# Optimization experiments

Hardware: AMD Instinct MI355X
Metric: run time of the kernel (lower is better)

The kernel has to match this reference:

```python
import jax, jax.numpy as jnp
import numpy as np

NUM_PARTS = 16
NUM_K = 256          # num_k_per_part; table rows per part = NUM_K + 1
VAE_DIMS = 768
OUT_DIMS = 1024
B = 4096


def setup_inputs() -> dict:
    key = jax.random.key(0)
    k0, k1, k2, k3, k4 = jax.random.split(key, 5)
    hashes = jax.random.randint(k0, (B, NUM_PARTS), 0, NUM_K + 1)  # values 0..256
    # nn.init.normal_(embedding.weight, 0.0, 0.01)
    emb = jax.random.normal(k1, ((NUM_K + 1) * NUM_PARTS, VAE_DIMS), dtype=jnp.float32) * 0.01
    # projection: Linear(768 -> 1024), ReLU, Linear(1024 -> 1024)
    W1 = jax.random.normal(k2, (VAE_DIMS, OUT_DIMS), dtype=jnp.float32) * (1.0 / np.sqrt(VAE_DIMS))
    b1 = jnp.zeros((OUT_DIMS,), dtype=jnp.float32)
    W2 = jax.random.normal(k3, (OUT_DIMS, OUT_DIMS), dtype=jnp.float32) * (1.0 / np.sqrt(OUT_DIMS))
    b2 = jnp.zeros((OUT_DIMS,), dtype=jnp.float32)
    # pe = randn(num_parts, out_dims) * 1.0
    pe = jax.random.normal(k4, (NUM_PARTS, OUT_DIMS), dtype=jnp.float32)
    return {"hashes": hashes, "emb": emb, "W1": W1, "b1": b1, "W2": W2, "b2": b2, "pe": pe}


def reference(hashes, emb, W1, b1, W2, b2, pe):
    # forward(hashes, index=None, get_mu=False, input_is_mu=False)
    offset = jnp.arange(NUM_PARTS, dtype=hashes.dtype) * (NUM_K + 1)  # [P]
    idx = hashes + offset[None, :]                                    # [B, P]
    mu = emb[idx]                                                     # [B, P, VAE]
    h = jax.nn.relu(jnp.einsum('bpv,vh->bph', mu, W1) + b1)           # [B, P, OUT]
    projected = jnp.einsum('bph,ho->bpo', h, W2) + b2                 # [B, P, OUT]
    return projected + pe[None, :, :]                                 # pe broadcast over batch
```

## Files before the change

### kernel.cpp

```cpp
#include <hip/hip_runtime.h>
#include <stdint.h>

#define NPARTS 16
#define NK1    257
#define ROWS   4112
#define MPAD   4224
#define VAE    768
#define ODIM   1024
#define BROWS  65536

typedef __attribute__((ext_vector_type(4))) float f32x4;
typedef __attribute__((ext_vector_type(8))) short s16x8;

static __device__ __forceinline__ unsigned short f2bf(float f) {
  union { float f; unsigned u; } v; v.f = f;
  unsigned x = v.u;
  unsigned r = x + 0x7FFFu + ((x >> 16) & 1u);
  return (unsigned short)(r >> 16);
}

static __device__ __forceinline__ void gload_lds16(const void* g, void* l) {
  __builtin_amdgcn_global_load_lds(
      (const __attribute__((address_space(1))) unsigned int*)g,
      (__attribute__((address_space(3))) unsigned int*)l, 16, 0, 0);
}

#define EMB_BLOCKS 1024
__global__ __launch_bounds__(256) void prep_kernel(
    const float* __restrict__ emb, const float* __restrict__ W1,
    unsigned short* __restrict__ embB, unsigned short* __restrict__ w1t) {
  __shared__ unsigned short tile[32][33];
  const int tid = threadIdx.x;
  const int bid = blockIdx.x;
  if (bid < EMB_BLOCKS) {
    const int NQ = MPAD * VAE / 4;
    for (int g = bid * 256 + tid; g < NQ; g += EMB_BLOCKS * 256) {
      const int i4 = g * 4;
      ushort4 o;
      if (i4 < ROWS * VAE) {
        const float4 v = *(const float4*)(emb + i4);
        o.x = f2bf(v.x); o.y = f2bf(v.y); o.z = f2bf(v.z); o.w = f2bf(v.w);
      } else {
        o.x = 0; o.y = 0; o.z = 0; o.w = 0;
      }
      *(ushort4*)(embB + i4) = o;
    }
  } else {
    const int tb = bid - EMB_BLOCKS;
    const int nkt = VAE / 32;
    const int tk = (tb % nkt) * 32;
    const int tn = (tb / nkt) * 32;
    const int r  = tid >> 3;
    const int c4 = (tid & 7) * 4;
    const float4 v = *(const float4*)(W1 + (size_t)(tk + r) * ODIM + tn + c4);
    tile[r][c4 + 0] = f2bf(v.x);
    tile[r][c4 + 1] = f2bf(v.y);
    tile[r][c4 + 2] = f2bf(v.z);
    tile[r][c4 + 3] = f2bf(v.w);
    __syncthreads();
    ushort4 o;
    o.x = tile[c4 + 0][r];
    o.y = tile[c4 + 1][r];
    o.z = tile[c4 + 2][r];
    o.w = tile[c4 + 3][r];
    *(ushort4*)(w1t + (size_t)(tn + r) * VAE + tk + c4) = o;
  }
}

template <int K, int MODE, bool DO_W2T>
__global__ __launch_bounds__(256) void gemm_kernel(
    const unsigned short* __restrict__ A, const unsigned short* __restrict__ BT,
    const float* __restrict__ bias, const float* __restrict__ pe,
    unsigned short* __restrict__ outB, float* __restrict__ outF,
    const float* __restrict__ W2src, unsigned short* __restrict__ w2dst) {
  __shared__ __align__(16) unsigned short smem[2 * 12288];
  const int tid = threadIdx.x;

  if (DO_W2T && blockIdx.z == 1) {
    if (blockIdx.y >= 32) return;
    unsigned short (*tile)[132] = (unsigned short (*)[132])smem;
    const int tk = blockIdx.y * 32, tn = blockIdx.x * 128;
#pragma unroll
    for (int p = 0; p < 4; ++p) {
      const int row = (tid >> 5) + p * 8, c4 = (tid & 31) * 4;
      const float4 v = *(const float4*)(W2src + (size_t)(tk + row) * ODIM + tn + c4);
      tile[row][c4 + 0] = f2bf(v.x); tile[row][c4 + 1] = f2bf(v.y);
      tile[row][c4 + 2] = f2bf(v.z); tile[row][c4 + 3] = f2bf(v.w);
    }
    __syncthreads();
#pragma unroll
    for (int q = 0; q < 4; ++q) {
      const int n = (tid >> 3) + q * 32, k4 = (tid & 7) * 4;
      ushort4 o;
      o.x = tile[k4 + 0][n]; o.y = tile[k4 + 1][n];
      o.z = tile[k4 + 2][n]; o.w = tile[k4 + 3][n];
      *(ushort4*)(w2dst + (size_t)(tn + n) * ODIM + tk + k4) = o;
    }
    return;
  }

  const int lane = tid & 63;
  const int wave = tid >> 6;
  const int wc   = wave * 32;
  const int brow = blockIdx.y * 64;
  const int bcol = blockIdx.x * 128;
  const int la   = lane & 15;
  const int hi   = lane >> 4;

  f32x4 acc[4][2];
#pragma unroll
  for (int m = 0; m < 4; ++m)
#pragma unroll
    for (int n = 0; n < 2; ++n)
#pragma unroll
      for (int r = 0; r < 4; ++r) acc[m][n][r] = 0.f;

  const int srow = tid >> 3;
  const int skb  = (tid & 7) ^ (srow & 7);
  const unsigned short* gA = A + (size_t)(brow + srow) * K + skb * 8;
  const unsigned short* gB = BT + (size_t)(bcol + srow) * K + skb * 8;

#define STAGE(b, kt)                                              \
  {                                                               \
    unsigned short* la_ = smem + (b) * 12288 + tid * 8;           \
    unsigned short* lb_ = la_ + 4096;                             \
    gload_lds16(gA + (kt), la_);                                  \
    gload_lds16(gA + (kt) + 32 * K, la_ + 2048);                  \
    gload_lds16(gB + (kt), lb_);                                  \
    gload_lds16(gB + (kt) + 32 * K, lb_ + 2048);                  \
    gload_lds16(gB + (kt) + 64 * K, lb_ + 4096);                  \
    gload_lds16(gB + (kt) + 96 * K, lb_ + 6144);                  \
  }

  STAGE(0, 0);
  asm volatile("s_waitcnt vmcnt(0)" ::: "memory");
  __builtin_amdgcn_s_barrier();

  const int NT = K / 64;
  for (int t = 0; t < NT; ++t) {
    const int cur = t & 1;
    if (t + 1 < NT) STAGE(cur ^ 1, (t + 1) * 64);

    const unsigned short* As = smem + cur * 12288;
    const unsigned short* Bs = As + 4096;
    s16x8 af[4][2], bf[2][2];
#pragma unroll
    for (int m = 0; m < 4; ++m)
#pragma unroll
      for (int ks = 0; ks < 2; ++ks)
        af[m][ks] = *(const s16x8*)(As + (m * 16 + la) * 64 +
                                    (((ks * 4 + hi) ^ (la & 7)) * 8));
#pragma unroll
    for (int n = 0; n < 2; ++n)
#pragma unroll
      for (int ks = 0; ks < 2; ++ks)
        bf[n][ks] = *(const s16x8*)(Bs + (wc + n * 16 + la) * 64 +
                                    (((ks * 4 + hi) ^ (la & 7)) * 8));
#pragma unroll
    for (int m = 0; m < 4; ++m)
#pragma unroll
      for (int n = 0; n < 2; ++n)
#pragma unroll
        for (int ks = 0; ks < 2; ++ks)
          acc[m][n] = __builtin_amdgcn_mfma_f32_16x16x32_bf16(af[m][ks], bf[n][ks],
                                                              acc[m][n], 0, 0, 0);
    asm volatile("s_waitcnt vmcnt(0)" ::: "memory");
    __builtin_amdgcn_sched_barrier(0);
    __builtin_amdgcn_s_barrier();
  }
#undef STAGE

#pragma unroll
  for (int m = 0; m < 4; ++m) {
    const int row0 = brow + m * 16 + hi * 4;
#pragma unroll
    for (int n = 0; n < 2; ++n) {
      const int col = bcol + wc + n * 16 + la;
      const float bv = bias[col];
      if (MODE == 0) {
#pragma unroll
        for (int r = 0; r < 4; ++r) {
          float v = acc[m][n][r] + bv;
          v = v > 0.f ? v : 0.f;
          outB[(size_t)(row0 + r) * ODIM + col] = f2bf(v);
        }
      } else {
#pragma unroll
        for (int r = 0; r < 4; ++r) {
          const int row = row0 + r;
          int p = row / NK1;
          if (p > NPARTS - 1) p = NPARTS - 1;
          outF[(size_t)row * ODIM + col] = acc[m][n][r] + bv + pe[(size_t)p * ODIM + col];
        }
      }
    }
  }
}

__global__ __launch_bounds__(256) void gather_kernel(const int* __restrict__ hashes,
                                                     const float* __restrict__ T,
                                                     float* __restrict__ out) {
  const int wid  = (blockIdx.x * blockDim.x + threadIdx.x) >> 6;
  const int lane = threadIdx.x & 63;
  const int nw   = (gridDim.x * blockDim.x) >> 6;
  for (int row = wid; row < BROWS; row += nw) {
    const int h = __builtin_amdgcn_readfirstlane(hashes[row]);
    const int p = row & (NPARTS - 1);
    const f32x4* __restrict__ src = (const f32x4*)(T + (size_t)(h + p * NK1) * ODIM);
    f32x4* __restrict__ dst = (f32x4*)(out + (size_t)row * ODIM);
#pragma unroll
    for (int j = 0; j < 4; ++j) {
      f32x4 v = src[lane + j * 64];
      __builtin_nontemporal_store(v, dst + lane + j * 64);
    }
  }
}

extern "C" void kernel_launch(void* const* d_in, const int* in_sizes, int n_in,
                              void* d_out, int out_size, void* d_ws, size_t ws_size,
                              hipStream_t stream) {
  const int*   hashes = (const int*)d_in[0];
  const float* emb    = (const float*)d_in[1];
  const float* W1     = (const float*)d_in[2];
  const float* b1     = (const float*)d_in[3];
  const float* W2     = (const float*)d_in[4];
  const float* b2     = (const float*)d_in[5];
  const float* pe     = (const float*)d_in[6];
  float* out = (float*)d_out;

  char* ws = (char*)d_ws;
  unsigned short* embB = (unsigned short*)(ws);
  unsigned short* w1t  = (unsigned short*)(ws + 6488064);
  unsigned short* w2t  = (unsigned short*)(ws + 8060928);
  unsigned short* H    = (unsigned short*)(ws + 10158080);
  float*          T    = (float*)(ws + 18808832);

  prep_kernel<<<EMB_BLOCKS + 768, 256, 0, stream>>>(emb, W1, embB, w1t);

  gemm_kernel<VAE, 0, true><<<dim3(8, 66, 2), 256, 0, stream>>>(
      embB, w1t, b1, nullptr, H, nullptr, W2, w2t);

  gemm_kernel<ODIM, 2, false><<<dim3(8, 66, 1), 256, 0, stream>>>(
      H, w2t, b2, pe, nullptr, T, nullptr, nullptr);

  gather_kernel<<<1024, 256, 0, stream>>>(hashes, T, out);
}
```

Measured before the change: 94.00 us.

## Fuse table gather into second GEMM epilogue via per-part hash bucketing

Builds per-part histograms and a bucketed row list of batch rows for each table entry inside the prep kernel. The second GEMM stages its output tile in shared memory and scatters each table row directly to every output row that references it. This removes the intermediate fp32 table write and the separate gather kernel's reread of it. It adds atomics, prefix scans, a per-row binary search and scattered stores in the epilogue.

```diff
diff --git a/kernel.cpp b/kernel.cpp
--- a/kernel.cpp
+++ b/kernel.cpp
@@ -8,6 +8,7 @@
 #define VAE    768
 #define ODIM   1024
 #define BROWS  65536
+#define BPART  4096
 
 typedef __attribute__((ext_vector_type(4))) float f32x4;
 typedef __attribute__((ext_vector_type(8))) short s16x8;
@@ -26,10 +27,14 @@
 }
 
 #define EMB_BLOCKS 1024
+#define W1_BLOCKS  768
 __global__ __launch_bounds__(256) void prep_kernel(
     const float* __restrict__ emb, const float* __restrict__ W1,
-    unsigned short* __restrict__ embB, unsigned short* __restrict__ w1t) {
+    const int* __restrict__ hashes,
+    unsigned short* __restrict__ embB, unsigned short* __restrict__ w1t,
+    int* __restrict__ gcnt, int* __restrict__ gbase, int* __restrict__ rowlist) {
   __shared__ unsigned short tile[32][33];
+  __shared__ int hist[512];
   const int tid = threadIdx.x;
   const int bid = blockIdx.x;
   if (bid < EMB_BLOCKS) {
@@ -45,7 +50,7 @@
       }
       *(ushort4*)(embB + i4) = o;
     }
-  } else {
+  } else if (bid < EMB_BLOCKS + W1_BLOCKS) {
     const int tb = bid - EMB_BLOCKS;
     const int nkt = VAE / 32;
     const int tk = (tb % nkt) * 32;
@@ -64,6 +69,41 @@
     o.z = tile[c4 + 2][r];
     o.w = tile[c4 + 3][r];
     *(ushort4*)(w1t + (size_t)(tn + r) * VAE + tk + c4) = o;
+  } else {
+    const int p = bid - (EMB_BLOCKS + W1_BLOCKS);
+    hist[tid] = 0; hist[tid + 256] = 0;
+    __syncthreads();
+    int hv[16];
+#pragma unroll
+    for (int u = 0; u < 16; ++u) {
+      const int b = u * 256 + tid;
+      hv[u] = hashes[b * NPARTS + p];
+      atomicAdd(&hist[hv[u]], 1);
+    }
+    __syncthreads();
+    const int o0 = hist[tid], o1 = hist[tid + 256];
+    for (int off = 1; off < 512; off <<= 1) {
+      const int v0 = (tid >= off) ? hist[tid - off] : 0;
+      const int v1 = hist[tid + 256 - off];
+      __syncthreads();
+      hist[tid] += v0; hist[tid + 256] += v1;
+      __syncthreads();
+    }
+    const int b0 = hist[tid] - o0;
+    const int b1 = hist[tid + 256] - o1;
+    gcnt[p * NK1 + tid]  = o0;
+    gbase[p * NK1 + tid] = b0;
+    if (tid == 0) { gcnt[p * NK1 + 256] = o1; gbase[p * NK1 + 256] = b1; }
+    if (p == 0 && tid < MPAD - ROWS) { gcnt[ROWS + tid] = 0; gbase[ROWS + tid] = 0; }
+    __syncthreads();
+    hist[tid] = b0; hist[tid + 256] = b1;
+    __syncthreads();
+#pragma unroll
+    for (int u = 0; u < 16; ++u) {
+      const int b = u * 256 + tid;
+      const int pos = atomicAdd(&hist[hv[u]], 1);
+      rowlist[p * BPART + pos] = b * NPARTS + p;
+    }
   }
 }
 
@@ -72,28 +112,30 @@
     const unsigned short* __restrict__ A, const unsigned short* __restrict__ BT,
     const float* __restrict__ bias, const float* __restrict__ pe,
     unsigned short* __restrict__ outB, float* __restrict__ outF,
-    const float* __restrict__ W2src, unsigned short* __restrict__ w2dst) {
+    const float* __restrict__ W2src, unsigned short* __restrict__ w2dst,
+    const int* __restrict__ gcnt, const int* __restrict__ gbase,
+    const int* __restrict__ rowlist) {
   __shared__ __align__(16) unsigned short smem[2 * 12288];
   const int tid = threadIdx.x;
 
   if (DO_W2T && blockIdx.z == 1) {
     if (blockIdx.y >= 32) return;
-    unsigned short (*tile)[132] = (unsigned short (*)[132])smem;
+    unsigned short (*ttile)[132] = (unsigned short (*)[132])smem;
     const int tk = blockIdx.y * 32, tn = blockIdx.x * 128;
 #pragma unroll
-    for (int p = 0; p < 4; ++p) {
-      const int row = (tid >> 5) + p * 8, c4 = (tid & 31) * 4;
+    for (int q = 0; q < 4; ++q) {
+      const int row = (tid >> 5) + q * 8, c4 = (tid & 31) * 4;
       const float4 v = *(const float4*)(W2src + (size_t)(tk + row) * ODIM + tn + c4);
-      tile[row][c4 + 0] = f2bf(v.x); tile[row][c4 + 1] = f2bf(v.y);
-      tile[row][c4 + 2] = f2bf(v.z); tile[row][c4 + 3] = f2bf(v.w);
+      ttile[row][c4 + 0] = f2bf(v.x); ttile[row][c4 + 1] = f2bf(v.y);
+      ttile[row][c4 + 2] = f2bf(v.z); ttile[row][c4 + 3] = f2bf(v.w);
     }
     __syncthreads();
 #pragma unroll
     for (int q = 0; q < 4; ++q) {
       const int n = (tid >> 3) + q * 32, k4 = (tid & 7) * 4;
       ushort4 o;
-      o.x = tile[k4 + 0][n]; o.y = tile[k4 + 1][n];
-      o.z = tile[k4 + 2][n]; o.w = tile[k4 + 3][n];
+      o.x = ttile[k4 + 0][n]; o.y = ttile[k4 + 1][n];
+      o.z = ttile[k4 + 2][n]; o.w = ttile[k4 + 3][n];
       *(ushort4*)(w2dst + (size_t)(tn + n) * ODIM + tk + k4) = o;
     }
     return;
@@ -170,48 +212,70 @@
   }
 #undef STAGE
 
-#pragma unroll
-  for (int m = 0; m < 4; ++m) {
-    const int row0 = brow + m * 16 + hi * 4;
-#pragma unroll
-    for (int n = 0; n < 2; ++n) {
-      const int col = bcol + wc + n * 16 + la;
-      const float bv = bias[col];
-      if (MODE == 0) {
+  if constexpr (MODE == 0) {
+#pragma unroll
+    for (int m = 0; m < 4; ++m) {
+      const int row0 = brow + m * 16 + hi * 4;
+#pragma unroll
+      for (int n = 0; n < 2; ++n) {
+        const int col = bcol + wc + n * 16 + la;
+        const float bv = bias[col];
 #pragma unroll
         for (int r = 0; r < 4; ++r) {
           float v = acc[m][n][r] + bv;
           v = v > 0.f ? v : 0.f;
           outB[(size_t)(row0 + r) * ODIM + col] = f2bf(v);
         }
-      } else {
+      }
+    }
+  } else {
+    __shared__ int pref[65];
+    __shared__ int cbase[64];
+    float (*tile)[128] = (float (*)[128])smem;
+#pragma unroll
+    for (int m = 0; m < 4; ++m) {
+      const int trl = m * 16 + hi * 4;
+#pragma unroll
+      for (int n = 0; n < 2; ++n) {
+        const int lcol = wc + n * 16 + la;
+        const int gcol = bcol + lcol;
+        const float bv = bias[gcol];
 #pragma unroll
         for (int r = 0; r < 4; ++r) {
-          const int row = row0 + r;
-          int p = row / NK1;
-          if (p > NPARTS - 1) p = NPARTS - 1;
-          outF[(size_t)row * ODIM + col] = acc[m][n][r] + bv + pe[(size_t)p * ODIM + col];
+          const int trow = brow + trl + r;
+          int p = trow / NK1; if (p > NPARTS - 1) p = NPARTS - 1;
+          tile[trl + r][lcol] = acc[m][n][r] + bv + pe[(size_t)p * ODIM + gcol];
         }
       }
     }
-  }
-}
-
-__global__ __launch_bounds__(256) void gather_kernel(const int* __restrict__ hashes,
-                                                     const float* __restrict__ T,
-                                                     float* __restrict__ out) {
-  const int wid  = (blockIdx.x * blockDim.x + threadIdx.x) >> 6;
-  const int lane = threadIdx.x & 63;
-  const int nw   = (gridDim.x * blockDim.x) >> 6;
-  for (int row = wid; row < BROWS; row += nw) {
-    const int h = __builtin_amdgcn_readfirstlane(hashes[row]);
-    const int p = row & (NPARTS - 1);
-    const f32x4* __restrict__ src = (const f32x4*)(T + (size_t)(h + p * NK1) * ODIM);
-    f32x4* __restrict__ dst = (f32x4*)(out + (size_t)row * ODIM);
-#pragma unroll
-    for (int j = 0; j < 4; ++j) {
-      f32x4 v = src[lane + j * 64];
-      __builtin_nontemporal_store(v, dst + lane + j * 64);
+    if (wave == 0) {
+      const int trow = brow + lane;
+      const int c = gcnt[trow];
+      int s = c;
+#pragma unroll
+      for (int off = 1; off < 64; off <<= 1) {
+        const int v = __shfl_up(s, off);
+        if (lane >= off) s += v;
+      }
+      pref[lane + 1] = s;
+      if (lane == 0) pref[0] = 0;
+      int p = trow / NK1; if (p > NPARTS - 1) p = NPARTS - 1;
+      cbase[lane] = p * BPART + gbase[trow];
+    }
+    __syncthreads();
+    const int Nit = pref[64];
+    const int hw  = wave * 2 + (lane >> 5);
+    const int l32 = lane & 31;
+    for (int iq = hw; iq < Nit; iq += 8) {
+      int lo = 0, hh = 64;
+      while (hh - lo > 1) {
+        const int mid = (lo + hh) >> 1;
+        if (pref[mid] <= iq) lo = mid; else hh = mid;
+      }
+      const int t = lo;
+      const int orow = rowlist[cbase[t] + (iq - pref[t])];
+      const f32x4 v = *(const f32x4*)&tile[t][l32 * 4];
+      __builtin_nontemporal_store(v, (f32x4*)(outF + (size_t)orow * ODIM + bcol + l32 * 4));
     }
   }
 }
@@ -233,15 +297,16 @@
   unsigned short* w1t  = (unsigned short*)(ws + 6488064);
   unsigned short* w2t  = (unsigned short*)(ws + 8060928);
   unsigned short* H    = (unsigned short*)(ws + 10158080);
-  float*          T    = (float*)(ws + 18808832);
-
-  prep_kernel<<<EMB_BLOCKS + 768, 256, 0, stream>>>(emb, W1, embB, w1t);
+  int*            gcnt = (int*)(ws + 18808832);
+  int*            gbas = (int*)(ws + 18825728);
+  int*            rowl = (int*)(ws + 18842624);
+
+  prep_kernel<<<EMB_BLOCKS + W1_BLOCKS + NPARTS, 256, 0, stream>>>(
+      emb, W1, hashes, embB, w1t, gcnt, gbas, rowl);
 
   gemm_kernel<VAE, 0, true><<<dim3(8, 66, 2), 256, 0, stream>>>(
-      embB, w1t, b1, nullptr, H, nullptr, W2, w2t);
+      embB, w1t, b1, nullptr, H, nullptr, W2, w2t, nullptr, nullptr, nullptr);
 
   gemm_kernel<ODIM, 2, false><<<dim3(8, 66, 1), 256, 0, stream>>>(
-      H, w2t, b2, pe, nullptr, T, nullptr, nullptr);
-
-  gather_kernel<<<1024, 256, 0, stream>>>(hashes, T, out);
-}
+      H, w2t, b2, pe, nullptr, out, nullptr, nullptr, gcnt, gbas, rowl);
+}
```

Result: slower. 127.6 us (+35.8%).

## Triple-buffer GEMM K-loop with partial vmcnt waits and MFMA priority

Applied to the files above, without the earlier changes.

The GEMM main loop moves from double to triple buffering of LDS tiles. Loads run two stages ahead, and the wait uses a partial vmcnt so one stage stays in flight while the current one is computed. It also raises wave priority around the MFMA block, fully unrolls the loop, and doubles the gather kernel grid. The cost targeted is exposed global-load latency in the GEMMs. In exchange, LDS use grows to 72KB per block, which may lower occupancy, and the unrolled loop increases code size.

```diff
diff --git a/kernel.cpp b/kernel.cpp
--- a/kernel.cpp
+++ b/kernel.cpp
@@ -73,27 +73,27 @@
     const float* __restrict__ bias, const float* __restrict__ pe,
     unsigned short* __restrict__ outB, float* __restrict__ outF,
     const float* __restrict__ W2src, unsigned short* __restrict__ w2dst) {
-  __shared__ __align__(16) unsigned short smem[2 * 12288];
+  __shared__ __align__(16) unsigned short smem[3 * 12288];
   const int tid = threadIdx.x;
 
   if (DO_W2T && blockIdx.z == 1) {
     if (blockIdx.y >= 32) return;
-    unsigned short (*tile)[132] = (unsigned short (*)[132])smem;
+    unsigned short (*ttile)[132] = (unsigned short (*)[132])smem;
     const int tk = blockIdx.y * 32, tn = blockIdx.x * 128;
 #pragma unroll
-    for (int p = 0; p < 4; ++p) {
-      const int row = (tid >> 5) + p * 8, c4 = (tid & 31) * 4;
+    for (int q = 0; q < 4; ++q) {
+      const int row = (tid >> 5) + q * 8, c4 = (tid & 31) * 4;
       const float4 v = *(const float4*)(W2src + (size_t)(tk + row) * ODIM + tn + c4);
-      tile[row][c4 + 0] = f2bf(v.x); tile[row][c4 + 1] = f2bf(v.y);
-      tile[row][c4 + 2] = f2bf(v.z); tile[row][c4 + 3] = f2bf(v.w);
+      ttile[row][c4 + 0] = f2bf(v.x); ttile[row][c4 + 1] = f2bf(v.y);
+      ttile[row][c4 + 2] = f2bf(v.z); ttile[row][c4 + 3] = f2bf(v.w);
     }
     __syncthreads();
 #pragma unroll
     for (int q = 0; q < 4; ++q) {
       const int n = (tid >> 3) + q * 32, k4 = (tid & 7) * 4;
       ushort4 o;
-      o.x = tile[k4 + 0][n]; o.y = tile[k4 + 1][n];
-      o.z = tile[k4 + 2][n]; o.w = tile[k4 + 3][n];
+      o.x = ttile[k4 + 0][n]; o.y = ttile[k4 + 1][n];
+      o.z = ttile[k4 + 2][n]; o.w = ttile[k4 + 3][n];
       *(ushort4*)(w2dst + (size_t)(tn + n) * ODIM + tk + k4) = o;
     }
     return;
@@ -132,16 +132,19 @@
     gload_lds16(gB + (kt) + 96 * K, lb_ + 6144);                  \
   }
 
+  const int NT = K / 64;
   STAGE(0, 0);
-  asm volatile("s_waitcnt vmcnt(0)" ::: "memory");
-  __builtin_amdgcn_s_barrier();
-
-  const int NT = K / 64;
+  STAGE(1, 64);
+
+#pragma unroll
   for (int t = 0; t < NT; ++t) {
-    const int cur = t & 1;
-    if (t + 1 < NT) STAGE(cur ^ 1, (t + 1) * 64);
-
-    const unsigned short* As = smem + cur * 12288;
+    if (t < NT - 1) asm volatile("s_waitcnt vmcnt(6)" ::: "memory");
+    else            asm volatile("s_waitcnt vmcnt(0)" ::: "memory");
+    __builtin_amdgcn_sched_barrier(0);
+    __builtin_amdgcn_s_barrier();
+    if (t + 2 < NT) STAGE((t + 2) % 3, (t + 2) * 64);
+
+    const unsigned short* As = smem + (t % 3) * 12288;
     const unsigned short* Bs = As + 4096;
     s16x8 af[4][2], bf[2][2];
 #pragma unroll
@@ -156,6 +159,10 @@
       for (int ks = 0; ks < 2; ++ks)
         bf[n][ks] = *(const s16x8*)(Bs + (wc + n * 16 + la) * 64 +
                                     (((ks * 4 + hi) ^ (la & 7)) * 8));
+    asm volatile("s_waitcnt lgkmcnt(0)" ::: "memory");
+    __builtin_amdgcn_sched_barrier(0);
+
+    __builtin_amdgcn_s_setprio(1);
 #pragma unroll
     for (int m = 0; m < 4; ++m)
 #pragma unroll
@@ -164,9 +171,7 @@
         for (int ks = 0; ks < 2; ++ks)
           acc[m][n] = __builtin_amdgcn_mfma_f32_16x16x32_bf16(af[m][ks], bf[n][ks],
                                                               acc[m][n], 0, 0, 0);
-    asm volatile("s_waitcnt vmcnt(0)" ::: "memory");
-    __builtin_amdgcn_sched_barrier(0);
-    __builtin_amdgcn_s_barrier();
+    __builtin_amdgcn_s_setprio(0);
   }
 #undef STAGE
 
@@ -243,5 +248,5 @@
   gemm_kernel<ODIM, 2, false><<<dim3(8, 66, 1), 256, 0, stream>>>(
       H, w2t, b2, pe, nullptr, T, nullptr, nullptr);
 
-  gather_kernel<<<1024, 256, 0, stream>>>(hashes, T, out);
-}
+  gather_kernel<<<2048, 256, 0, stream>>>(hashes, T, out);
+}
```

Measured after the change: 95.36 us. Within noise of the previous version (+1.5%).

## Store projected table in bf16 and gather with XCD-local part partitioning

Applied to the files above, without the earlier changes.

The second GEMM now writes the per-part projected table as bf16 instead of fp32, halving its write and the gather's read traffic. The gather kernel expands bf16 back to fp32 on load. It also assigns blocks so that each XCD handles only two parts, which keeps each XCD's slice of the table resident in its local L2. This adds an extra bf16 rounding of the final output, which raises the error relative to the fp32 reference.

```diff
diff --git a/kernel.cpp b/kernel.cpp
--- a/kernel.cpp
+++ b/kernel.cpp
@@ -17,6 +17,11 @@
   unsigned x = v.u;
   unsigned r = x + 0x7FFFu + ((x >> 16) & 1u);
   return (unsigned short)(r >> 16);
+}
+
+static __device__ __forceinline__ float bf2f(unsigned short s) {
+  union { unsigned u; float f; } v; v.u = ((unsigned)s) << 16;
+  return v.f;
 }
 
 static __device__ __forceinline__ void gload_lds16(const void* g, void* l) {
@@ -71,29 +76,29 @@
 __global__ __launch_bounds__(256) void gemm_kernel(
     const unsigned short* __restrict__ A, const unsigned short* __restrict__ BT,
     const float* __restrict__ bias, const float* __restrict__ pe,
-    unsigned short* __restrict__ outB, float* __restrict__ outF,
+    unsigned short* __restrict__ outB,
     const float* __restrict__ W2src, unsigned short* __restrict__ w2dst) {
   __shared__ __align__(16) unsigned short smem[2 * 12288];
   const int tid = threadIdx.x;
 
   if (DO_W2T && blockIdx.z == 1) {
     if (blockIdx.y >= 32) return;
-    unsigned short (*tile)[132] = (unsigned short (*)[132])smem;
+    unsigned short (*ttile)[132] = (unsigned short (*)[132])smem;
     const int tk = blockIdx.y * 32, tn = blockIdx.x * 128;
 #pragma unroll
-    for (int p = 0; p < 4; ++p) {
-      const int row = (tid >> 5) + p * 8, c4 = (tid & 31) * 4;
+    for (int q = 0; q < 4; ++q) {
+      const int row = (tid >> 5) + q * 8, c4 = (tid & 31) * 4;
       const float4 v = *(const float4*)(W2src + (size_t)(tk + row) * ODIM + tn + c4);
-      tile[row][c4 + 0] = f2bf(v.x); tile[row][c4 + 1] = f2bf(v.y);
-      tile[row][c4 + 2] = f2bf(v.z); tile[row][c4 + 3] = f2bf(v.w);
+      ttile[row][c4 + 0] = f2bf(v.x); ttile[row][c4 + 1] = f2bf(v.y);
+      ttile[row][c4 + 2] = f2bf(v.z); ttile[row][c4 + 3] = f2bf(v.w);
     }
     __syncthreads();
 #pragma unroll
     for (int q = 0; q < 4; ++q) {
       const int n = (tid >> 3) + q * 32, k4 = (tid & 7) * 4;
       ushort4 o;
-      o.x = tile[k4 + 0][n]; o.y = tile[k4 + 1][n];
-      o.z = tile[k4 + 2][n]; o.w = tile[k4 + 3][n];
+      o.x = ttile[k4 + 0][n]; o.y = ttile[k4 + 1][n];
+      o.z = ttile[k4 + 2][n]; o.w = ttile[k4 + 3][n];
       *(ushort4*)(w2dst + (size_t)(tn + n) * ODIM + tk + k4) = o;
     }
     return;
@@ -190,7 +195,8 @@
           const int row = row0 + r;
           int p = row / NK1;
           if (p > NPARTS - 1) p = NPARTS - 1;
-          outF[(size_t)row * ODIM + col] = acc[m][n][r] + bv + pe[(size_t)p * ODIM + col];
+          outB[(size_t)row * ODIM + col] =
+              f2bf(acc[m][n][r] + bv + pe[(size_t)p * ODIM + col]);
         }
       }
     }
@@ -198,20 +204,35 @@
 }
 
 __global__ __launch_bounds__(256) void gather_kernel(const int* __restrict__ hashes,
-                                                     const float* __restrict__ T,
+                                                     const unsigned short* __restrict__ Tb,
                                                      float* __restrict__ out) {
-  const int wid  = (blockIdx.x * blockDim.x + threadIdx.x) >> 6;
+  const int xcd  = blockIdx.x & 7;
+  const int bi   = blockIdx.x >> 3;
+  const int wave = threadIdx.x >> 6;
   const int lane = threadIdx.x & 63;
-  const int nw   = (gridDim.x * blockDim.x) >> 6;
-  for (int row = wid; row < BROWS; row += nw) {
-    const int h = __builtin_amdgcn_readfirstlane(hashes[row]);
-    const int p = row & (NPARTS - 1);
-    const f32x4* __restrict__ src = (const f32x4*)(T + (size_t)(h + p * NK1) * ODIM);
-    f32x4* __restrict__ dst = (f32x4*)(out + (size_t)row * ODIM);
-#pragma unroll
-    for (int j = 0; j < 4; ++j) {
-      f32x4 v = src[lane + j * 64];
-      __builtin_nontemporal_store(v, dst + lane + j * 64);
+  const int wl   = bi * 4 + wave;
+  const int p0   = xcd * 2;
+#pragma unroll
+  for (int i = 0; i < 8; ++i) {
+    const int r     = wl + i * 1024;
+    const int batch = r >> 1;
+    const int p     = p0 + (r & 1);
+    const int orow  = batch * NPARTS + p;
+    const int h = __builtin_amdgcn_readfirstlane(hashes[orow]);
+    const unsigned short* srcrow = Tb + (size_t)(h + p * NK1) * ODIM;
+    float* dstrow = out + (size_t)orow * ODIM;
+#pragma unroll
+    for (int half = 0; half < 2; ++half) {
+      const int e0 = half * 512 + lane * 8;
+      const s16x8 v = *(const s16x8*)(srcrow + e0);
+      f32x4 lo, hh;
+#pragma unroll
+      for (int j = 0; j < 4; ++j) {
+        lo[j] = bf2f((unsigned short)v[j]);
+        hh[j] = bf2f((unsigned short)v[j + 4]);
+      }
+      __builtin_nontemporal_store(lo, (f32x4*)(dstrow + e0));
+      __builtin_nontemporal_store(hh, (f32x4*)(dstrow + e0 + 4));
     }
   }
 }
@@ -233,15 +254,15 @@
   unsigned short* w1t  = (unsigned short*)(ws + 6488064);
   unsigned short* w2t  = (unsigned short*)(ws + 8060928);
   unsigned short* H    = (unsigned short*)(ws + 10158080);
-  float*          T    = (float*)(ws + 18808832);
+  unsigned short* Tb   = (unsigned short*)(ws + 18808832);
 
   prep_kernel<<<EMB_BLOCKS + 768, 256, 0, stream>>>(emb, W1, embB, w1t);
 
   gemm_kernel<VAE, 0, true><<<dim3(8, 66, 2), 256, 0, stream>>>(
-      embB, w1t, b1, nullptr, H, nullptr, W2, w2t);
+      embB, w1t, b1, nullptr, H, W2, w2t);
 
   gemm_kernel<ODIM, 2, false><<<dim3(8, 66, 1), 256, 0, stream>>>(
-      H, w2t, b2, pe, nullptr, T, nullptr, nullptr);
-
-  gather_kernel<<<1024, 256, 0, stream>>>(hashes, T, out);
-}
+      H, w2t, b2, pe, Tb, nullptr, nullptr);
+
+  gather_kernel<<<2048, 256, 0, stream>>>(hashes, Tb, out);
+}
```

Result: slower. 162.1 us (+72.4%).
